# Kernel optimization log

Measured on AMD Instinct MI355X. Metric: run time of the kernel, lower is better.

The kernel has to match this reference:

```python
import jax, jax.numpy as jnp
import numpy as np

N_NODES = 50000
N_EDGES = 600000
N_FEAT = 128
HIDDEN = 128
OUT_CH = 128
N_GRAPHS = 64
BN_EPS = 1e-5


def gcn_conv(x, src, dst, ew, W, b):
    """PyG GCNConv: add self-loops, symmetric deg^{-1/2} normalization with edge weights."""
    n = x.shape[0]
    h = x @ W  # [N, out]
    loop = jnp.arange(n)
    src2 = jnp.concatenate([src, loop])
    dst2 = jnp.concatenate([dst, loop])
    w2 = jnp.concatenate([ew, jnp.ones((n,), x.dtype)])
    deg = jax.ops.segment_sum(w2, dst2, num_segments=n)
    dinv = jnp.where(deg > 0, jax.lax.rsqrt(deg), 0.0)
    norm = dinv[src2] * w2 * dinv[dst2]  # [E+N]
    out = jax.ops.segment_sum(h[src2] * norm[:, None], dst2, num_segments=n)
    return out + b


def setup_inputs() -> dict:
    key = jax.random.key(0)
    ks = jax.random.split(key, 12)
    x = jax.random.normal(ks[0], (N_NODES, N_FEAT), jnp.float32)
    edge_index = jax.random.randint(ks[1], (2, N_EDGES), 0, N_NODES, dtype=jnp.int64)
    batch = jnp.sort(jax.random.randint(ks[2], (N_NODES,), 0, N_GRAPHS, dtype=jnp.int64))
    edge_attr = jax.random.uniform(ks[3], (N_EDGES,), jnp.float32)
    s1 = 1.0 / np.sqrt(N_FEAT)
    s2 = 1.0 / np.sqrt(HIDDEN)
    s3 = 1.0 / np.sqrt(OUT_CH)
    s4 = 1.0 / np.sqrt(OUT_CH // 2)
    return {
        "x": x, "edge_index": edge_index, "batch": batch, "edge_attr": edge_attr,
        "W1": jax.random.uniform(ks[4], (N_FEAT, HIDDEN), jnp.float32, -s1, s1),
        "b1": jnp.zeros((HIDDEN,), jnp.float32),
        "W2": jax.random.uniform(ks[5], (HIDDEN, OUT_CH), jnp.float32, -s2, s2),
        "b2": jnp.zeros((OUT_CH,), jnp.float32),
        "fc1_W": jax.random.uniform(ks[6], (OUT_CH, OUT_CH // 2), jnp.float32, -s3, s3),
        "fc1_b": jax.random.uniform(ks[7], (OUT_CH // 2,), jnp.float32, -s3, s3),
        "bn_gamma": jnp.ones((OUT_CH // 2,), jnp.float32),
        "bn_beta": jnp.zeros((OUT_CH // 2,), jnp.float32),
        "fc3_W": jax.random.uniform(ks[8], (OUT_CH // 2, 1), jnp.float32, -s4, s4),
        "fc3_b": jax.random.uniform(ks[9], (1,), jnp.float32, -s4, s4),
    }


def reference(x, edge_index, batch, edge_attr, W1, b1, W2, b2,
              fc1_W, fc1_b, bn_gamma, bn_beta, fc3_W, fc3_b):
    src, dst = edge_index[0], edge_index[1]
    h = jax.nn.relu(gcn_conv(x, src, dst, edge_attr, W1, b1))
    # dropout skipped (deterministic eval: mode=False)
    h = jax.nn.relu(gcn_conv(h, src, dst, edge_attr, W2, b2))
    # global_mean_pool over batch segment ids
    sums = jax.ops.segment_sum(h, batch, num_segments=N_GRAPHS)  # [G, out]
    cnt = jax.ops.segment_sum(jnp.ones_like(batch, jnp.float32), batch, num_segments=N_GRAPHS)
    g = sums / jnp.maximum(cnt, 1.0)[:, None]
    z = jax.nn.relu(g @ fc1_W + fc1_b)
    # BatchNorm1d with batch statistics (training-mode math, biased var)
    mean = jnp.mean(z, axis=0)
    var = jnp.mean((z - mean) ** 2, axis=0)
    z = bn_gamma * (z - mean) * jax.lax.rsqrt(var + BN_EPS) + bn_beta
    return z @ fc3_W + fc3_b  # [G, 1]
```

## Files before the change

kernel.cpp:

```cpp
#include <hip/hip_runtime.h>

#define NNODES 50000
#define NEDGES 600000
#define NGRAPHS 64
#define BN_EPS 1e-5f
#define NB1 ((NNODES + 255) / 256)
#define PPG 16
#define GEMM_BLOCKS ((NNODES + 127) / 128)
#define NOWN 64
#define RANGE 782
#define SEG 16
#define SEGI4 (NEDGES / SEG / 4)
#define HIST_BLOCKS (NOWN * SEG)


__device__ __forceinline__ void gemm_tile(const float* __restrict__ A,
        const float* __restrict__ W, float* __restrict__ C, int block) {
    __shared__ float a_lds[16][132];
    __shared__ float w_lds[16][192];
    const int tid = threadIdx.x;
    const int row0 = block * 128;
    const int tx = tid & 15;
    const int ty = tid >> 4;
    float acc[4][8];
#pragma unroll
    for (int i = 0; i < 4; ++i)
#pragma unroll
        for (int j = 0; j < 8; ++j) acc[i][j] = 0.f;

    for (int kc = 0; kc < 128; kc += 16) {
        {
            int r = tid >> 2;
            int k4 = (tid & 3) << 2;
            int grow = row0 + r;
            float4 v = make_float4(0.f, 0.f, 0.f, 0.f);
            if (grow < NNODES) v = *(const float4*)(A + (size_t)grow * 128 + kc + k4);
            a_lds[k4 + 0][r] = v.x; a_lds[k4 + 1][r] = v.y;
            a_lds[k4 + 2][r] = v.z; a_lds[k4 + 3][r] = v.w;
        }
        {
            int kk = tid >> 5;
            int c4 = tid & 31;
            float4 v = *(const float4*)(W + (size_t)(kc + kk) * 128 + c4 * 4);
            int sw = 12 * (c4 >> 1) + ((c4 & 1) << 2);
            *(float4*)&w_lds[kk][sw] = v;
        }
        __syncthreads();
#pragma unroll
        for (int k = 0; k < 16; ++k) {
            float a[4], b[8];
            *(float4*)&a[0] = *(const float4*)&a_lds[k][ty * 4];
            *(float4*)&b[0] = *(const float4*)&w_lds[k][tx * 12];
            *(float4*)&b[4] = *(const float4*)&w_lds[k][tx * 12 + 4];
#pragma unroll
            for (int i = 0; i < 4; ++i)
#pragma unroll
                for (int j = 0; j < 8; ++j)
                    acc[i][j] = fmaf(a[i], b[j], acc[i][j]);
        }
        __syncthreads();
    }
#pragma unroll
    for (int i = 0; i < 4; ++i) {
        int grow = row0 + ty * 4 + i;
        if (grow < NNODES) {
            float4 v0 = make_float4(acc[i][0], acc[i][1], acc[i][2], acc[i][3]);
            float4 v1 = make_float4(acc[i][4], acc[i][5], acc[i][6], acc[i][7]);
            *(float4*)(C + (size_t)grow * 128 + tx * 8) = v0;
            *(float4*)(C + (size_t)grow * 128 + tx * 8 + 4) = v1;
        }
    }
}

__global__ __launch_bounds__(512) void k_gemm1_hist(const float* __restrict__ A,
        const float* __restrict__ W, float* __restrict__ C,
        const int* __restrict__ dst, int* __restrict__ cnt_seg) {
    if (blockIdx.x >= GEMM_BLOCKS) {
        __shared__ int lh[RANGE];
        int t = threadIdx.x;
        int hb = blockIdx.x - GEMM_BLOCKS;
        int own = hb & (NOWN - 1);
        int seg = hb >> 6;
        int lo = own * RANGE;
        int n = min(RANGE, NNODES - lo);
        for (int i = t; i < RANGE; i += 512) lh[i] = 0;
        __syncthreads();
        const int4* d4 = (const int4*)dst;
        int q1 = (seg + 1) * SEGI4;
        for (int q = seg * SEGI4 + t; q < q1; q += 512) {
            int4 v = d4[q];
            unsigned a0 = (unsigned)(v.x - lo);
            unsigned a1 = (unsigned)(v.y - lo);
            unsigned a2 = (unsigned)(v.z - lo);
            unsigned a3 = (unsigned)(v.w - lo);
            if (a0 < (unsigned)n) atomicAdd(&lh[a0], 1);
            if (a1 < (unsigned)n) atomicAdd(&lh[a1], 1);
            if (a2 < (unsigned)n) atomicAdd(&lh[a2], 1);
            if (a3 < (unsigned)n) atomicAdd(&lh[a3], 1);
        }
        __syncthreads();
        for (int i = t; i < n; i += 512) cnt_seg[(size_t)seg * NNODES + lo + i] = lh[i];
        return;
    }
    gemm_tile(A, W, C, blockIdx.x);
}

__global__ __launch_bounds__(512) void k_gemm(const float* __restrict__ A,
        const float* __restrict__ W, float* __restrict__ C) {
    gemm_tile(A, W, C, blockIdx.x);
}


__global__ __launch_bounds__(256) void k_scan1(const int* __restrict__ cnt_seg,
        int* __restrict__ excl, int* __restrict__ bsum) {
    __shared__ int sh[256];
    int b = blockIdx.x, t = threadIdx.x;
    int idx = b * 256 + t;
    int v = 0;
    if (idx < NNODES) {
#pragma unroll
        for (int s = 0; s < SEG; ++s) v += cnt_seg[(size_t)s * NNODES + idx];
    }
    sh[t] = v;
    __syncthreads();
#pragma unroll
    for (int off = 1; off < 256; off <<= 1) {
        int x = (t >= off) ? sh[t - off] : 0;
        __syncthreads();
        sh[t] += x;
        __syncthreads();
    }
    if (idx < NNODES) excl[idx] = sh[t] - v;
    if (t == 255) bsum[b] = sh[255];
}

__global__ __launch_bounds__(256) void k_scan2(int* __restrict__ bsum) {
    __shared__ int sh[256];
    int t = threadIdx.x;
    int v = (t < NB1) ? bsum[t] : 0;
    sh[t] = v;
    __syncthreads();
#pragma unroll
    for (int off = 1; off < 256; off <<= 1) {
        int x = (t >= off) ? sh[t - off] : 0;
        __syncthreads();
        sh[t] += x;
        __syncthreads();
    }
    if (t < NB1) bsum[t] = sh[t] - v;
}

__global__ __launch_bounds__(256) void k_scan3base(const int* __restrict__ excl,
        const int* __restrict__ bsum, const int* __restrict__ cnt_seg,
        int* __restrict__ row_start, int* __restrict__ base) {
    int b = blockIdx.x, t = threadIdx.x;
    int idx = b * 256 + t;
    if (idx >= NNODES) return;
    int rs = excl[idx] + bsum[b];
    row_start[idx] = rs;
    if (idx == 0) row_start[NNODES] = NEDGES;
    int run = rs;
#pragma unroll
    for (int s = 0; s < SEG; ++s) {
        int c = cnt_seg[(size_t)s * NNODES + idx];
        base[(size_t)s * NNODES + idx] = run;
        run += c;
    }
}


__global__ __launch_bounds__(512) void k_place_seg(const int* __restrict__ dst,
        const int* __restrict__ src, const float* __restrict__ ew,
        const int* __restrict__ base, int2* __restrict__ csr_pk) {
    __shared__ int lh[RANGE];
    int t = threadIdx.x;
    int own = blockIdx.x & (NOWN - 1);
    int seg = blockIdx.x >> 6;
    int lo = own * RANGE;
    int n = min(RANGE, NNODES - lo);
    for (int i = t; i < RANGE; i += 512) lh[i] = 0;
    __syncthreads();
    const int4* d4 = (const int4*)dst;
    int q1 = (seg + 1) * SEGI4;
    for (int q = seg * SEGI4 + t; q < q1; q += 512) {
        int4 v = d4[q];
        int e = q * 4;
        unsigned a0 = (unsigned)(v.x - lo);
        unsigned a1 = (unsigned)(v.y - lo);
        unsigned a2 = (unsigned)(v.z - lo);
        unsigned a3 = (unsigned)(v.w - lo);
        if (a0 < (unsigned)n) {
            int tk = atomicAdd(&lh[a0], 1);
            csr_pk[base[(size_t)seg * NNODES + v.x] + tk] =
                make_int2(src[e], __float_as_int(ew[e]));
        }
        if (a1 < (unsigned)n) {
            int tk = atomicAdd(&lh[a1], 1);
            csr_pk[base[(size_t)seg * NNODES + v.y] + tk] =
                make_int2(src[e + 1], __float_as_int(ew[e + 1]));
        }
        if (a2 < (unsigned)n) {
            int tk = atomicAdd(&lh[a2], 1);
            csr_pk[base[(size_t)seg * NNODES + v.z] + tk] =
                make_int2(src[e + 2], __float_as_int(ew[e + 2]));
        }
        if (a3 < (unsigned)n) {
            int tk = atomicAdd(&lh[a3], 1);
            csr_pk[base[(size_t)seg * NNODES + v.w] + tk] =
                make_int2(src[e + 3], __float_as_int(ew[e + 3]));
        }
    }
}

__global__ __launch_bounds__(256) void k_deg(const int* __restrict__ row_start,
        const int2* __restrict__ csr_pk, float* __restrict__ dinv) {
    int i = blockIdx.x * 256 + threadIdx.x;
    if (i >= NNODES) return;
    int e0 = row_start[i], e1 = row_start[i + 1];
    float deg = 1.f;
    for (int e = e0; e < e1; ++e) deg += __int_as_float(csr_pk[e].y);
    dinv[i] = rsqrtf(deg);
}

__global__ __launch_bounds__(256) void k_wfill(const int* __restrict__ row_start,
        int2* __restrict__ csr_pk, const float* __restrict__ dinv) {
    int i = blockIdx.x * 256 + threadIdx.x;
    if (i >= NNODES) return;
    int e0 = row_start[i], e1 = row_start[i + 1];
    float di = dinv[i];
    for (int e = e0; e < e1; ++e) {
        int2 pk = csr_pk[e];
        float w = dinv[pk.x] * __int_as_float(pk.y) * di;
        csr_pk[e].y = __float_as_int(w);
    }
}


__global__ __launch_bounds__(256) void k_aggregate(const float* __restrict__ h,
        const float* __restrict__ dinv, const int* __restrict__ row_start,
        const int2* __restrict__ csr_pk, const float* __restrict__ bias,
        float* __restrict__ out) {
    int gtid = blockIdx.x * 256 + threadIdx.x;
    int i = gtid >> 5;
    int lane = (gtid & 31) << 2;
    if (i >= NNODES) return;
    float di = dinv[i];
    float sw = di * di;
    float4 hv = *(const float4*)(h + (size_t)i * 128 + lane);
    float ax = sw * hv.x, ay = sw * hv.y, az = sw * hv.z, aw = sw * hv.w;
    int e = row_start[i];
    int e1 = row_start[i + 1];
    for (; e + 3 < e1; e += 4) {
        int2 p0 = csr_pk[e], p1 = csr_pk[e + 1], p2 = csr_pk[e + 2], p3 = csr_pk[e + 3];
        float4 v0 = *(const float4*)(h + (size_t)p0.x * 128 + lane);
        float4 v1 = *(const float4*)(h + (size_t)p1.x * 128 + lane);
        float4 v2 = *(const float4*)(h + (size_t)p2.x * 128 + lane);
        float4 v3 = *(const float4*)(h + (size_t)p3.x * 128 + lane);
        float w0 = __int_as_float(p0.y), w1 = __int_as_float(p1.y);
        float w2 = __int_as_float(p2.y), w3 = __int_as_float(p3.y);
        ax = fmaf(w0, v0.x, ax); ay = fmaf(w0, v0.y, ay);
        az = fmaf(w0, v0.z, az); aw = fmaf(w0, v0.w, aw);
        ax = fmaf(w1, v1.x, ax); ay = fmaf(w1, v1.y, ay);
        az = fmaf(w1, v1.z, az); aw = fmaf(w1, v1.w, aw);
        ax = fmaf(w2, v2.x, ax); ay = fmaf(w2, v2.y, ay);
        az = fmaf(w2, v2.z, az); aw = fmaf(w2, v2.w, aw);
        ax = fmaf(w3, v3.x, ax); ay = fmaf(w3, v3.y, ay);
        az = fmaf(w3, v3.z, az); aw = fmaf(w3, v3.w, aw);
    }
    for (; e < e1; ++e) {
        int2 p0 = csr_pk[e];
        float w0 = __int_as_float(p0.y);
        float4 v0 = *(const float4*)(h + (size_t)p0.x * 128 + lane);
        ax = fmaf(w0, v0.x, ax); ay = fmaf(w0, v0.y, ay);
        az = fmaf(w0, v0.z, az); aw = fmaf(w0, v0.w, aw);
    }
    float4 b = *(const float4*)(bias + lane);
    float4 o;
    o.x = fmaxf(ax + b.x, 0.f);
    o.y = fmaxf(ay + b.y, 0.f);
    o.z = fmaxf(az + b.z, 0.f);
    o.w = fmaxf(aw + b.w, 0.f);
    *(float4*)(out + (size_t)i * 128 + lane) = o;
}


__global__ __launch_bounds__(256) void k_pool1(const float* __restrict__ h2,
        const int* __restrict__ batch, float* __restrict__ part) {
    __shared__ float sh[256];
    int g = blockIdx.x / PPG;
    int p = blockIdx.x % PPG;
    int t = threadIdx.x;
    int lo = 0, hi = NNODES;
    while (lo < hi) { int mid = (lo + hi) >> 1; if (batch[mid] < g) lo = mid + 1; else hi = mid; }
    int b0 = lo;
    lo = 0; hi = NNODES;
    int g1 = g + 1;
    while (lo < hi) { int mid = (lo + hi) >> 1; if (batch[mid] < g1) lo = mid + 1; else hi = mid; }
    int b1 = lo;

    int c = t & 127, q = t >> 7;
    float acc = 0.f;
    for (int r = b0 + p * 2 + q; r < b1; r += PPG * 2) acc += h2[(size_t)r * 128 + c];
    sh[t] = acc;
    __syncthreads();
    if (t < 128) part[((size_t)g * PPG + p) * 128 + t] = sh[t] + sh[t + 128];
}

__global__ __launch_bounds__(128) void k_pool2(const float* __restrict__ part,
        const int* __restrict__ batch, float* __restrict__ gmean) {
    int g = blockIdx.x;
    int t = threadIdx.x;
    int lo = 0, hi = NNODES;
    while (lo < hi) { int mid = (lo + hi) >> 1; if (batch[mid] < g) lo = mid + 1; else hi = mid; }
    int b0 = lo;
    lo = 0; hi = NNODES;
    int g1 = g + 1;
    while (lo < hi) { int mid = (lo + hi) >> 1; if (batch[mid] < g1) lo = mid + 1; else hi = mid; }
    int b1 = lo;
    float s = 0.f;
#pragma unroll
    for (int p = 0; p < PPG; ++p) s += part[((size_t)g * PPG + p) * 128 + t];
    float n = (float)(b1 - b0);
    gmean[g * 128 + t] = s / fmaxf(n, 1.f);
}


__global__ __launch_bounds__(256) void k_head(const float* __restrict__ gmean,
        const float* __restrict__ fc1W, const float* __restrict__ fc1b,
        const float* __restrict__ gamma, const float* __restrict__ beta,
        const float* __restrict__ fc3W, const float* __restrict__ fc3b,
        float* __restrict__ out) {
    __shared__ float g[64][129];
    __shared__ float w[128][64];
    __shared__ float z[64][65];
    __shared__ float mu[64], isd[64];
    int t = threadIdx.x;
#pragma unroll
    for (int p = 0; p < 8; ++p) {
        int idx4 = p * 256 + t;
        int gg = idx4 >> 5;
        int c4 = (idx4 & 31) << 2;
        float4 v = *(const float4*)(gmean + gg * 128 + c4);
        *(float4*)&g[gg][c4] = v;
    }
#pragma unroll
    for (int p = 0; p < 8; ++p) {
        int idx4 = p * 256 + t;
        float4 v = *(const float4*)(fc1W + idx4 * 4);
        ((float4*)&w[0][0])[idx4] = v;
    }
    __syncthreads();
    int r = t >> 2;
    int c0 = (t & 3) * 16;
    float acc[16];
#pragma unroll
    for (int j = 0; j < 16; ++j) acc[j] = 0.f;
    for (int k = 0; k < 128; ++k) {
        float gv = g[r][k];
#pragma unroll
        for (int j = 0; j < 16; ++j) acc[j] = fmaf(gv, w[k][c0 + j], acc[j]);
    }
#pragma unroll
    for (int j = 0; j < 16; ++j)
        z[r][c0 + j] = fmaxf(acc[j] + fc1b[c0 + j], 0.f);
    __syncthreads();
    if (t < 64) {
        float m = 0.f;
        for (int rr = 0; rr < 64; ++rr) m += z[rr][t];
        m *= (1.f / 64.f);
        float v = 0.f;
        for (int rr = 0; rr < 64; ++rr) { float d = z[rr][t] - m; v = fmaf(d, d, v); }
        v *= (1.f / 64.f);
        mu[t] = m;
        isd[t] = rsqrtf(v + BN_EPS);
    }
    __syncthreads();
    if (t < 64) {
        float a2 = fc3b[0];
        for (int cc = 0; cc < 64; ++cc) {
            float zn = fmaf(gamma[cc] * (z[t][cc] - mu[cc]), isd[cc], beta[cc]);
            a2 = fmaf(zn, fc3W[cc], a2);
        }
        out[t] = a2;
    }
}


extern "C" void kernel_launch(void* const* d_in, const int* in_sizes, int n_in,
                              void* d_out, int out_size, void* d_ws, size_t ws_size,
                              hipStream_t stream) {
    const float* x    = (const float*)d_in[0];
    const int*   ei   = (const int*)d_in[1];
    const int*   batch= (const int*)d_in[2];
    const float* ew   = (const float*)d_in[3];
    const float* W1   = (const float*)d_in[4];
    const float* b1   = (const float*)d_in[5];
    const float* W2   = (const float*)d_in[6];
    const float* b2   = (const float*)d_in[7];
    const float* fc1W = (const float*)d_in[8];
    const float* fc1b = (const float*)d_in[9];
    const float* gam  = (const float*)d_in[10];
    const float* bet  = (const float*)d_in[11];
    const float* fc3W = (const float*)d_in[12];
    const float* fc3b = (const float*)d_in[13];
    float* out = (float*)d_out;
    const int* srcp = ei;
    const int* dstp = ei + NEDGES;

    char* wsb = (char*)d_ws;
    size_t off = 0;
    auto alloc = [&](size_t bytes) {
        void* p = wsb + off;
        off = (off + bytes + 255) & ~(size_t)255;
        return p;
    };
    float* dinv      = (float*)alloc(NNODES * 4);
    int*   row_start = (int*)alloc((NNODES + 1) * 4);
    int*   cnt_seg   = (int*)alloc((size_t)SEG * NNODES * 4);
    int*   base      = (int*)alloc((size_t)SEG * NNODES * 4);
    int*   excl      = (int*)alloc(NNODES * 4);
    int*   bsum      = (int*)alloc(NB1 * 4);
    int2*  csr_pk    = (int2*)alloc((size_t)NEDGES * 8);
    float* hbuf      = (float*)alloc((size_t)NNODES * 128 * 4);
    float* abuf      = (float*)alloc((size_t)NNODES * 128 * 4);
    float* part      = (float*)alloc((size_t)NGRAPHS * PPG * 128 * 4);
    float* gmean     = (float*)alloc(NGRAPHS * 128 * 4);
    (void)ws_size; (void)in_sizes; (void)n_in; (void)out_size;

    k_gemm1_hist<<<GEMM_BLOCKS + HIST_BLOCKS, 512, 0, stream>>>(x, W1, hbuf, dstp, cnt_seg);
    k_scan1<<<NB1, 256, 0, stream>>>(cnt_seg, excl, bsum);
    k_scan2<<<1, 256, 0, stream>>>(bsum);
    k_scan3base<<<NB1, 256, 0, stream>>>(excl, bsum, cnt_seg, row_start, base);
    k_place_seg<<<HIST_BLOCKS, 512, 0, stream>>>(dstp, srcp, ew, base, csr_pk);
    k_deg<<<NB1, 256, 0, stream>>>(row_start, csr_pk, dinv);
    k_wfill<<<NB1, 256, 0, stream>>>(row_start, csr_pk, dinv);

    k_aggregate<<<(NNODES * 32 + 255) / 256, 256, 0, stream>>>(hbuf, dinv, row_start,
                                                               csr_pk, b1, abuf);
    k_gemm<<<GEMM_BLOCKS, 512, 0, stream>>>(abuf, W2, hbuf);
    k_aggregate<<<(NNODES * 32 + 255) / 256, 256, 0, stream>>>(hbuf, dinv, row_start,
                                                               csr_pk, b2, abuf);
    k_pool1<<<NGRAPHS * PPG, 256, 0, stream>>>(abuf, batch, part);
    k_pool2<<<NGRAPHS, 128, 0, stream>>>(part, batch, gmean);
    k_head<<<1, 256, 0, stream>>>(gmean, fc1W, fc1b, gam, bet, fc3W, fc3b, out);
}
```

Before: 242.1 us.

## Fold degree computation into histogram and normalize edge weights during CSR placement

The histogram blocks now also accumulate per-segment edge-weight sums in LDS, so the scan kernel can compute deg^{-1/2} directly. The placement kernel writes fully normalized weights, which removes the separate k_deg and k_wfill passes over the CSR array and two launches. The aggregate kernel also gains an 8-way unrolled gather loop to keep more loads in flight. In exchange it adds float LDS atomics and an extra segmented buffer, and the per-node degree sum order changes, so float rounding can differ slightly.

```diff
diff --git a/kernel.cpp b/kernel.cpp
--- a/kernel.cpp
+++ b/kernel.cpp
@@ -74,32 +74,39 @@
 
 __global__ __launch_bounds__(512) void k_gemm1_hist(const float* __restrict__ A,
         const float* __restrict__ W, float* __restrict__ C,
-        const int* __restrict__ dst, int* __restrict__ cnt_seg) {
+        const int* __restrict__ dst, const float* __restrict__ ew,
+        int* __restrict__ cnt_seg, float* __restrict__ ewsum_seg) {
     if (blockIdx.x >= GEMM_BLOCKS) {
         __shared__ int lh[RANGE];
+        __shared__ float lew[RANGE];
         int t = threadIdx.x;
         int hb = blockIdx.x - GEMM_BLOCKS;
         int own = hb & (NOWN - 1);
         int seg = hb >> 6;
         int lo = own * RANGE;
         int n = min(RANGE, NNODES - lo);
-        for (int i = t; i < RANGE; i += 512) lh[i] = 0;
+        for (int i = t; i < RANGE; i += 512) { lh[i] = 0; lew[i] = 0.f; }
         __syncthreads();
         const int4* d4 = (const int4*)dst;
+        const float4* w4 = (const float4*)ew;
         int q1 = (seg + 1) * SEGI4;
         for (int q = seg * SEGI4 + t; q < q1; q += 512) {
             int4 v = d4[q];
+            float4 wv = w4[q];
             unsigned a0 = (unsigned)(v.x - lo);
             unsigned a1 = (unsigned)(v.y - lo);
             unsigned a2 = (unsigned)(v.z - lo);
             unsigned a3 = (unsigned)(v.w - lo);
-            if (a0 < (unsigned)n) atomicAdd(&lh[a0], 1);
-            if (a1 < (unsigned)n) atomicAdd(&lh[a1], 1);
-            if (a2 < (unsigned)n) atomicAdd(&lh[a2], 1);
-            if (a3 < (unsigned)n) atomicAdd(&lh[a3], 1);
-        }
-        __syncthreads();
-        for (int i = t; i < n; i += 512) cnt_seg[(size_t)seg * NNODES + lo + i] = lh[i];
+            if (a0 < (unsigned)n) { atomicAdd(&lh[a0], 1); atomicAdd(&lew[a0], wv.x); }
+            if (a1 < (unsigned)n) { atomicAdd(&lh[a1], 1); atomicAdd(&lew[a1], wv.y); }
+            if (a2 < (unsigned)n) { atomicAdd(&lh[a2], 1); atomicAdd(&lew[a2], wv.z); }
+            if (a3 < (unsigned)n) { atomicAdd(&lh[a3], 1); atomicAdd(&lew[a3], wv.w); }
+        }
+        __syncthreads();
+        for (int i = t; i < n; i += 512) {
+            cnt_seg[(size_t)seg * NNODES + lo + i] = lh[i];
+            ewsum_seg[(size_t)seg * NNODES + lo + i] = lew[i];
+        }
         return;
     }
     gemm_tile(A, W, C, blockIdx.x);
@@ -152,7 +159,8 @@
 
 __global__ __launch_bounds__(256) void k_scan3base(const int* __restrict__ excl,
         const int* __restrict__ bsum, const int* __restrict__ cnt_seg,
-        int* __restrict__ row_start, int* __restrict__ base) {
+        const float* __restrict__ ewsum_seg, int* __restrict__ row_start,
+        int* __restrict__ base, float* __restrict__ dinv) {
     int b = blockIdx.x, t = threadIdx.x;
     int idx = b * 256 + t;
     if (idx >= NNODES) return;
@@ -160,25 +168,33 @@
     row_start[idx] = rs;
     if (idx == 0) row_start[NNODES] = NEDGES;
     int run = rs;
+    float deg = 1.f;
 #pragma unroll
     for (int s = 0; s < SEG; ++s) {
         int c = cnt_seg[(size_t)s * NNODES + idx];
         base[(size_t)s * NNODES + idx] = run;
         run += c;
-    }
-}
-
-
-__global__ __launch_bounds__(512) void k_place_seg(const int* __restrict__ dst,
+        deg += ewsum_seg[(size_t)s * NNODES + idx];
+    }
+    dinv[idx] = rsqrtf(deg);
+}
+
+
+__global__ __launch_bounds__(512) void k_place_final(const int* __restrict__ dst,
         const int* __restrict__ src, const float* __restrict__ ew,
-        const int* __restrict__ base, int2* __restrict__ csr_pk) {
+        const int* __restrict__ base, const float* __restrict__ dinv,
+        int2* __restrict__ csr_pk) {
     __shared__ int lh[RANGE];
+    __shared__ float ldinv[RANGE];
     int t = threadIdx.x;
     int own = blockIdx.x & (NOWN - 1);
     int seg = blockIdx.x >> 6;
     int lo = own * RANGE;
     int n = min(RANGE, NNODES - lo);
-    for (int i = t; i < RANGE; i += 512) lh[i] = 0;
+    for (int i = t; i < RANGE; i += 512) {
+        lh[i] = 0;
+        ldinv[i] = (i < n) ? dinv[lo + i] : 0.f;
+    }
     __syncthreads();
     const int4* d4 = (const int4*)dst;
     int q1 = (seg + 1) * SEGI4;
@@ -191,47 +207,28 @@
         unsigned a3 = (unsigned)(v.w - lo);
         if (a0 < (unsigned)n) {
             int tk = atomicAdd(&lh[a0], 1);
-            csr_pk[base[(size_t)seg * NNODES + v.x] + tk] =
-                make_int2(src[e], __float_as_int(ew[e]));
+            int s = src[e];
+            float w = dinv[s] * ew[e] * ldinv[a0];
+            csr_pk[base[(size_t)seg * NNODES + v.x] + tk] = make_int2(s, __float_as_int(w));
         }
         if (a1 < (unsigned)n) {
             int tk = atomicAdd(&lh[a1], 1);
-            csr_pk[base[(size_t)seg * NNODES + v.y] + tk] =
-                make_int2(src[e + 1], __float_as_int(ew[e + 1]));
+            int s = src[e + 1];
+            float w = dinv[s] * ew[e + 1] * ldinv[a1];
+            csr_pk[base[(size_t)seg * NNODES + v.y] + tk] = make_int2(s, __float_as_int(w));
         }
         if (a2 < (unsigned)n) {
             int tk = atomicAdd(&lh[a2], 1);
-            csr_pk[base[(size_t)seg * NNODES + v.z] + tk] =
-                make_int2(src[e + 2], __float_as_int(ew[e + 2]));
+            int s = src[e + 2];
+            float w = dinv[s] * ew[e + 2] * ldinv[a2];
+            csr_pk[base[(size_t)seg * NNODES + v.z] + tk] = make_int2(s, __float_as_int(w));
         }
         if (a3 < (unsigned)n) {
             int tk = atomicAdd(&lh[a3], 1);
-            csr_pk[base[(size_t)seg * NNODES + v.w] + tk] =
-                make_int2(src[e + 3], __float_as_int(ew[e + 3]));
-        }
-    }
-}
-
-__global__ __launch_bounds__(256) void k_deg(const int* __restrict__ row_start,
-        const int2* __restrict__ csr_pk, float* __restrict__ dinv) {
-    int i = blockIdx.x * 256 + threadIdx.x;
-    if (i >= NNODES) return;
-    int e0 = row_start[i], e1 = row_start[i + 1];
-    float deg = 1.f;
-    for (int e = e0; e < e1; ++e) deg += __int_as_float(csr_pk[e].y);
-    dinv[i] = rsqrtf(deg);
-}
-
-__global__ __launch_bounds__(256) void k_wfill(const int* __restrict__ row_start,
-        int2* __restrict__ csr_pk, const float* __restrict__ dinv) {
-    int i = blockIdx.x * 256 + threadIdx.x;
-    if (i >= NNODES) return;
-    int e0 = row_start[i], e1 = row_start[i + 1];
-    float di = dinv[i];
-    for (int e = e0; e < e1; ++e) {
-        int2 pk = csr_pk[e];
-        float w = dinv[pk.x] * __int_as_float(pk.y) * di;
-        csr_pk[e].y = __float_as_int(w);
+            int s = src[e + 3];
+            float w = dinv[s] * ew[e + 3] * ldinv[a3];
+            csr_pk[base[(size_t)seg * NNODES + v.w] + tk] = make_int2(s, __float_as_int(w));
+        }
     }
 }
 
@@ -250,6 +247,21 @@
     float ax = sw * hv.x, ay = sw * hv.y, az = sw * hv.z, aw = sw * hv.w;
     int e = row_start[i];
     int e1 = row_start[i + 1];
+    for (; e + 7 < e1; e += 8) {
+        int2 p[8];
+        float4 v[8];
+#pragma unroll
+        for (int j = 0; j < 8; ++j) p[j] = csr_pk[e + j];
+#pragma unroll
+        for (int j = 0; j < 8; ++j)
+            v[j] = *(const float4*)(h + (size_t)p[j].x * 128 + lane);
+#pragma unroll
+        for (int j = 0; j < 8; ++j) {
+            float w = __int_as_float(p[j].y);
+            ax = fmaf(w, v[j].x, ax); ay = fmaf(w, v[j].y, ay);
+            az = fmaf(w, v[j].z, az); aw = fmaf(w, v[j].w, aw);
+        }
+    }
     for (; e + 3 < e1; e += 4) {
         int2 p0 = csr_pk[e], p1 = csr_pk[e + 1], p2 = csr_pk[e + 2], p3 = csr_pk[e + 3];
         float4 v0 = *(const float4*)(h + (size_t)p0.x * 128 + lane);
@@ -417,6 +429,7 @@
     float* dinv      = (float*)alloc(NNODES * 4);
     int*   row_start = (int*)alloc((NNODES + 1) * 4);
     int*   cnt_seg   = (int*)alloc((size_t)SEG * NNODES * 4);
+    float* ewsum_seg = (float*)alloc((size_t)SEG * NNODES * 4);
     int*   base      = (int*)alloc((size_t)SEG * NNODES * 4);
     int*   excl      = (int*)alloc(NNODES * 4);
     int*   bsum      = (int*)alloc(NB1 * 4);
@@ -427,13 +440,13 @@
     float* gmean     = (float*)alloc(NGRAPHS * 128 * 4);
     (void)ws_size; (void)in_sizes; (void)n_in; (void)out_size;
 
-    k_gemm1_hist<<<GEMM_BLOCKS + HIST_BLOCKS, 512, 0, stream>>>(x, W1, hbuf, dstp, cnt_seg);
+    k_gemm1_hist<<<GEMM_BLOCKS + HIST_BLOCKS, 512, 0, stream>>>(x, W1, hbuf, dstp, ew,
+                                                                cnt_seg, ewsum_seg);
     k_scan1<<<NB1, 256, 0, stream>>>(cnt_seg, excl, bsum);
     k_scan2<<<1, 256, 0, stream>>>(bsum);
-    k_scan3base<<<NB1, 256, 0, stream>>>(excl, bsum, cnt_seg, row_start, base);
-    k_place_seg<<<HIST_BLOCKS, 512, 0, stream>>>(dstp, srcp, ew, base, csr_pk);
-    k_deg<<<NB1, 256, 0, stream>>>(row_start, csr_pk, dinv);
-    k_wfill<<<NB1, 256, 0, stream>>>(row_start, csr_pk, dinv);
+    k_scan3base<<<NB1, 256, 0, stream>>>(excl, bsum, cnt_seg, ewsum_seg,
+                                         row_start, base, dinv);
+    k_place_final<<<HIST_BLOCKS, 512, 0, stream>>>(dstp, srcp, ew, base, dinv, csr_pk);
 
     k_aggregate<<<(NNODES * 32 + 255) / 256, 256, 0, stream>>>(hbuf, dinv, row_start,
                                                                csr_pk, b1, abuf);
```

After: 252.5 us. 1.04x slower.
